# Performance work log

Hardware: AMD Instinct MI355X
Metric: run time of the kernel (lower is better)

## Reference

```python
import jax, jax.numpy as jnp
import numpy as np


def setup_inputs() -> dict:
    key = jax.random.key(0)
    k1, k2, k3 = jax.random.split(key, 3)
    B, S, IN, OUT = 4, 2048, 4096, 4096
    # int8 activations, weights, bias (stored as int8; math accumulates in int32)
    x = jax.random.randint(k1, (B, S, IN), -127, 128, dtype=jnp.int32).astype(jnp.int8)
    weight = jax.random.randint(k2, (OUT, IN), -127, 128, dtype=jnp.int32).astype(jnp.int8)  # (out, in)
    bias = jax.random.randint(k3, (1, OUT), -127, 128, dtype=jnp.int32).astype(jnp.int8)
    alpha = jnp.float32(0.001)  # input_scale*weight_scale/output_scale
    beta = jnp.float32(0.01)    # bias_scale/output_scale
    return {"x": x, "weight": weight, "bias": bias, "alpha": alpha, "beta": beta}


def reference(x, weight, bias, alpha, beta):
    # Flatten leading dims: (B,S,IN) -> (N,IN)
    x_shape = x.shape
    xf = x.reshape(-1, x_shape[-1])
    acc = jax.lax.dot_general(
        xf, weight,
        dimension_numbers=(((1,), (1,)), ((), ())),
        preferred_element_type=jnp.int32,
    )  # (N, OUT) int32
    # Fused epilogue: y = round(alpha*acc + beta*bias), saturate to int8
    yf = alpha * acc.astype(jnp.float32) + beta * bias.astype(jnp.float32)
    y = jnp.clip(jnp.round(yf), -128.0, 127.0).astype(jnp.int8)
    return y.reshape(*x_shape[:-1], -1)
```

## Files before the change

### kernel.cpp

```cpp
#include <hip/hip_runtime.h>
#include <stdint.h>

using i32x4  = __attribute__((ext_vector_type(4)))  int;
using i32x16 = __attribute__((ext_vector_type(16))) int;

#define M_TOT 8192
#define N_TOT 4096
#define K_TOT 4096
#define BM 256
#define BN 256

__device__ __forceinline__ void gload_lds16(const void* g, void* l) {
  __builtin_amdgcn_global_load_lds(
      (const __attribute__((address_space(1))) void*)(uintptr_t)g,
      (__attribute__((address_space(3))) void*)(uint32_t)(uintptr_t)l,
      16, 0, 0);
}

__global__ void pack_tiles(const int* __restrict__ a32, const int* __restrict__ b32,
                           int8_t* __restrict__ ap, int8_t* __restrict__ bp,
                           int na, int ntot) {
  int stride = gridDim.x * blockDim.x;
  for (int idx = blockIdx.x * blockDim.x + threadIdx.x; idx < ntot; idx += stride) {
    int i = idx;
    const int* src;
    int8_t* dst;
    if (idx < na) { src = a32; dst = ap; }
    else          { src = b32; dst = bp; i = idx - na; }
    int sp = i & 3;
    int rr = (i >> 2) & 255;
    int kc = (i >> 10) & 63;
    int p  = i >> 16;
    int sl = sp ^ ((rr >> 1) & 3);
    const i32x4* s = (const i32x4*)(src + (((size_t)(p * 256 + rr)) << 12) + kc * 64 + sl * 16);
    i32x4 a = s[0], b = s[1], c = s[2], d = s[3];
    i32x4 o;
    o.x = (a.x & 255) | ((a.y & 255) << 8) | ((a.z & 255) << 16) | (a.w << 24);
    o.y = (b.x & 255) | ((b.y & 255) << 8) | ((b.z & 255) << 16) | (b.w << 24);
    o.z = (c.x & 255) | ((c.y & 255) << 8) | ((c.z & 255) << 16) | (c.w << 24);
    o.w = (d.x & 255) | ((d.y & 255) << 8) | ((d.z & 255) << 16) | (d.w << 24);
    ((i32x4*)dst)[i] = o;
  }
}

#define STAGE_A(KC, SLOT) {                                                 \
    const int8_t* _g = Asrc + (size_t)(KC) * 16384 + stoff;                 \
    char* _d = lds + (SLOT) * 16384 + stoff;                                \
    gload_lds16(_g, _d); gload_lds16(_g + 8192, _d + 8192); }
#define STAGE_B(KC, SLOT) {                                                 \
    const int8_t* _g = Bsrc + (size_t)(KC) * 16384 + stoff;                 \
    char* _d = lds + 32768 + (SLOT) * 16384 + stoff;                        \
    gload_lds16(_g, _d); gload_lds16(_g + 8192, _d + 8192); }

#define LOAD_SET(FA, FB, SLOT, KS) {                                        \
    const char* _pa = lds + (SLOT) * 16384 + kOff[KS];                      \
    const char* _pb = _pa + 32768;                                          \
    FA[0] = *(const i32x4*)(_pa + aRow[0]);                                 \
    FA[1] = *(const i32x4*)(_pa + aRow[1]);                                 \
    FA[2] = *(const i32x4*)(_pa + aRow[2]);                                 \
    FA[3] = *(const i32x4*)(_pa + aRow[3]);                                 \
    FB[0] = *(const i32x4*)(_pb + bRow[0]);                                 \
    FB[1] = *(const i32x4*)(_pb + bRow[1]); }

#define MFMA8(FA, FB)                                                       \
    _Pragma("unroll")                                                       \
    for (int mi = 0; mi < 4; ++mi)                                          \
    _Pragma("unroll")                                                       \
    for (int ni = 0; ni < 2; ++ni)                                          \
      acc[mi][ni] = __builtin_amdgcn_mfma_i32_32x32x32_i8(FA[mi], FB[ni], acc[mi][ni], 0, 0, 0);

#define KTILE(SA_, SB_, SC_, SLOT, KC2, DO_STAGE, DO_NEXT) {                \
    LOAD_SET(fA##SB_, fB##SB_, SLOT, 1)                                     \
    asm volatile("s_waitcnt vmcnt(0)" ::: "memory");                        \
    __builtin_amdgcn_s_barrier();                                           \
    __builtin_amdgcn_sched_barrier(0);                                      \
    if (DO_STAGE) { STAGE_A(KC2, SLOT) STAGE_B(KC2, SLOT) }                 \
    __builtin_amdgcn_s_setprio(1);                                          \
    MFMA8(fA##SA_, fB##SA_)                                                 \
    __builtin_amdgcn_s_setprio(0);                                          \
    if (DO_NEXT) LOAD_SET(fA##SC_, fB##SC_, (SLOT) ^ 1, 0)                  \
    __builtin_amdgcn_s_setprio(1);                                          \
    MFMA8(fA##SB_, fB##SB_)                                                 \
    __builtin_amdgcn_s_setprio(0); }

__global__ __launch_bounds__(512, 2) void gemm_w8a8(
    const int8_t* __restrict__ Apack,
    const int8_t* __restrict__ Bpack,
    const int*    __restrict__ bias,
    const float*  __restrict__ alphap,
    const float*  __restrict__ betap,
    int* __restrict__ out)
{
  __shared__ __align__(16) char lds[65536];

  const int bid = blockIdx.x;
  const int xcd = bid & 7, wi = bid >> 3;
  const int tm = (xcd & 3) * 8 + (wi & 7);
  const int tn = (xcd >> 2) * 8 + (wi >> 3);

  const int tid = threadIdx.x;
  const int w   = tid >> 6;
  const int l   = tid & 63;
  const int lr  = l & 31;
  const int hi  = l >> 5;
  const int wr  = w >> 2;
  const int wc  = w & 3;
  const int stoff = tid * 16;

  const int8_t* Asrc = Apack + ((size_t)tm << 20);
  const int8_t* Bsrc = Bpack + ((size_t)tn << 20);

  const int swz = (lr >> 1) & 3;
  int aRow[4], bRow[2], kOff[2];
#pragma unroll
  for (int mi = 0; mi < 4; ++mi) aRow[mi] = (wr * 128 + mi * 32 + lr) * 64;
#pragma unroll
  for (int ni = 0; ni < 2; ++ni) bRow[ni] = (wc * 64 + ni * 32 + lr) * 64;
#pragma unroll
  for (int ks = 0; ks < 2; ++ks) kOff[ks] = ((((ks << 1) | hi)) ^ swz) * 16;

  i32x16 acc[4][2] = {};
  i32x4 fA0[4], fB0[2], fA1[4], fB1[2], fA2[4], fB2[2];

  STAGE_A(0, 0) STAGE_B(0, 0)
  STAGE_A(1, 1) STAGE_B(1, 1)
  asm volatile("s_waitcnt vmcnt(4)" ::: "memory");
  __builtin_amdgcn_s_barrier();
  __builtin_amdgcn_sched_barrier(0);
  LOAD_SET(fA0, fB0, 0, 0)

  for (int t = 0; t < 10; ++t) {
    const int kk = t * 6;
    KTILE(0, 1, 2, 0, kk + 2, 1, 1)
    KTILE(2, 0, 1, 1, kk + 3, 1, 1)
    KTILE(1, 2, 0, 0, kk + 4, 1, 1)
    KTILE(0, 1, 2, 1, kk + 5, 1, 1)
    KTILE(2, 0, 1, 0, kk + 6, 1, 1)
    KTILE(1, 2, 0, 1, kk + 7, 1, 1)
  }
  KTILE(0, 1, 2, 0, 62, 1, 1)
  KTILE(2, 0, 1, 1, 63, 1, 1)
  KTILE(1, 2, 0, 0, 0,  0, 1)
  KTILE(0, 1, 2, 1, 0,  0, 0)

  const float alpha = *alphap;
  const float beta  = *betap;
  const int brow = tm * BM, bcol = tn * BN;
#pragma unroll
  for (int ni = 0; ni < 2; ++ni) {
    const int col = bcol + wc * 64 + ni * 32 + lr;
    const float bb = beta * (float)bias[col];
#pragma unroll
    for (int mi = 0; mi < 4; ++mi) {
      const int rbase = brow + wr * 128 + mi * 32 + 4 * hi;
#pragma unroll
      for (int r = 0; r < 16; ++r) {
        const int row = rbase + (r & 3) + 8 * (r >> 2);
        float v = alpha * (float)acc[mi][ni][r] + bb;
        v = rintf(v);
        v = fminf(127.f, fmaxf(-128.f, v));
        out[(size_t)row * N_TOT + col] = (int)v;
      }
    }
  }
}

extern "C" void kernel_launch(void* const* d_in, const int* in_sizes, int n_in,
                              void* d_out, int out_size, void* d_ws, size_t ws_size,
                              hipStream_t stream) {
  const int*   x32    = (const int*)d_in[0];
  const int*   w32    = (const int*)d_in[1];
  const int*   bias   = (const int*)d_in[2];
  const float* alphap = (const float*)d_in[3];
  const float* betap  = (const float*)d_in[4];
  int* out = (int*)d_out;

  int8_t* xp = (int8_t*)d_ws;
  int8_t* wp = xp + (size_t)M_TOT * K_TOT;

  const int na   = (M_TOT * K_TOT) / 16;
  const int ntot = na + (N_TOT * K_TOT) / 16;
  pack_tiles<<<3072, 256, 0, stream>>>(x32, w32, xp, wp, na, ntot);

  gemm_w8a8<<<512, 512, 0, stream>>>(xp, wp, bias, alphap, betap, out);
}
```

Measured before the change: 197.5 us.

## Split warps into two phase-offset groups with triple-buffered LDS staging

Moves LDS staging from a double buffer to a triple buffer and regroups the 8 waves into two parity groups of four. One group loads its whole k-tile fragments from LDS and then runs MFMAs. The other group runs MFMAs on fragments it prefetched during the previous interval and then loads the next tile. The aim is to keep the matrix units busy by having one group issue LDS reads while the other computes. It raises LDS use to 96KB per block and changes the per-wave tile mapping, which could cut occupancy or add register pressure, and the divergent per-wave schedule may not line up as intended.

```diff
diff --git a/kernel.cpp b/kernel.cpp
--- a/kernel.cpp
+++ b/kernel.cpp
@@ -43,45 +43,45 @@
   }
 }
 
-#define STAGE_A(KC, SLOT) {                                                 \
-    const int8_t* _g = Asrc + (size_t)(KC) * 16384 + stoff;                 \
-    char* _d = lds + (SLOT) * 16384 + stoff;                                \
-    gload_lds16(_g, _d); gload_lds16(_g + 8192, _d + 8192); }
-#define STAGE_B(KC, SLOT) {                                                 \
-    const int8_t* _g = Bsrc + (size_t)(KC) * 16384 + stoff;                 \
-    char* _d = lds + 32768 + (SLOT) * 16384 + stoff;                        \
-    gload_lds16(_g, _d); gload_lds16(_g + 8192, _d + 8192); }
+#define STAGE_AB(KC, SLOT) {                                                \
+    const int8_t* _ga = Asrc + (size_t)(KC) * 16384 + stoff;                \
+    char* _da = lds + (SLOT) * 16384 + stoff;                               \
+    gload_lds16(_ga, _da); gload_lds16(_ga + 8192, _da + 8192);             \
+    const int8_t* _gb = Bsrc + (size_t)(KC) * 16384 + stoff;                \
+    char* _db = lds + 49152 + (SLOT) * 16384 + stoff;                       \
+    gload_lds16(_gb, _db); gload_lds16(_gb + 8192, _db + 8192); }
 
-#define LOAD_SET(FA, FB, SLOT, KS) {                                        \
-    const char* _pa = lds + (SLOT) * 16384 + kOff[KS];                      \
-    const char* _pb = _pa + 32768;                                          \
-    FA[0] = *(const i32x4*)(_pa + aRow[0]);                                 \
-    FA[1] = *(const i32x4*)(_pa + aRow[1]);                                 \
-    FA[2] = *(const i32x4*)(_pa + aRow[2]);                                 \
-    FA[3] = *(const i32x4*)(_pa + aRow[3]);                                 \
-    FB[0] = *(const i32x4*)(_pb + bRow[0]);                                 \
-    FB[1] = *(const i32x4*)(_pb + bRow[1]); }
+#define LOAD_TILE(FA, FB, SLOT) {                                           \
+    const char* _p0 = lds + (SLOT) * 16384;                                 \
+    _Pragma("unroll") for (int ks = 0; ks < 2; ++ks) {                      \
+      _Pragma("unroll") for (int mi = 0; mi < 4; ++mi)                      \
+        FA[ks][mi] = *(const i32x4*)(_p0 + aRow[mi] + kOff[ks]);            \
+      _Pragma("unroll") for (int ni = 0; ni < 2; ++ni)                      \
+        FB[ks][ni] = *(const i32x4*)(_p0 + 49152 + bRow[ni] + kOff[ks]);    \
+    } }
 
-#define MFMA8(FA, FB)                                                       \
-    _Pragma("unroll")                                                       \
-    for (int mi = 0; mi < 4; ++mi)                                          \
-    _Pragma("unroll")                                                       \
-    for (int ni = 0; ni < 2; ++ni)                                          \
-      acc[mi][ni] = __builtin_amdgcn_mfma_i32_32x32x32_i8(FA[mi], FB[ni], acc[mi][ni], 0, 0, 0);
+#define MFMA16(FA, FB)                                                      \
+    _Pragma("unroll") for (int ks = 0; ks < 2; ++ks)                        \
+    _Pragma("unroll") for (int mi = 0; mi < 4; ++mi)                        \
+    _Pragma("unroll") for (int ni = 0; ni < 2; ++ni)                        \
+      acc[mi][ni] = __builtin_amdgcn_mfma_i32_32x32x32_i8(FA[ks][mi], FB[ks][ni], acc[mi][ni], 0, 0, 0);
 
-#define KTILE(SA_, SB_, SC_, SLOT, KC2, DO_STAGE, DO_NEXT) {                \
-    LOAD_SET(fA##SB_, fB##SB_, SLOT, 1)                                     \
+#define INTERVAL(SLOT, NSLOT, SP, SR, KC2, DO_STAGE, DO_AHEAD) {            \
     asm volatile("s_waitcnt vmcnt(0)" ::: "memory");                        \
     __builtin_amdgcn_s_barrier();                                           \
     __builtin_amdgcn_sched_barrier(0);                                      \
-    if (DO_STAGE) { STAGE_A(KC2, SLOT) STAGE_B(KC2, SLOT) }                 \
-    __builtin_amdgcn_s_setprio(1);                                          \
-    MFMA8(fA##SA_, fB##SA_)                                                 \
-    __builtin_amdgcn_s_setprio(0);                                          \
-    if (DO_NEXT) LOAD_SET(fA##SC_, fB##SC_, (SLOT) ^ 1, 0)                  \
-    __builtin_amdgcn_s_setprio(1);                                          \
-    MFMA8(fA##SB_, fB##SB_)                                                 \
-    __builtin_amdgcn_s_setprio(0); }
+    if (DO_STAGE) STAGE_AB(KC2, (KC2) % 3)                                  \
+    if (!par) {                                                             \
+      LOAD_TILE(fA##SP, fB##SP, SLOT)                                       \
+      __builtin_amdgcn_s_setprio(1);                                        \
+      MFMA16(fA##SP, fB##SP)                                                \
+      __builtin_amdgcn_s_setprio(0);                                        \
+    } else {                                                                \
+      __builtin_amdgcn_s_setprio(1);                                        \
+      MFMA16(fA##SP, fB##SP)                                                \
+      __builtin_amdgcn_s_setprio(0);                                        \
+      if (DO_AHEAD) LOAD_TILE(fA##SR, fB##SR, NSLOT)                        \
+    } }
 
 __global__ __launch_bounds__(512, 2) void gemm_w8a8(
     const int8_t* __restrict__ Apack,
@@ -91,7 +91,7 @@
     const float*  __restrict__ betap,
     int* __restrict__ out)
 {
-  __shared__ __align__(16) char lds[65536];
+  __shared__ __align__(16) char lds[98304];
 
   const int bid = blockIdx.x;
   const int xcd = bid & 7, wi = bid >> 3;
@@ -103,8 +103,9 @@
   const int l   = tid & 63;
   const int lr  = l & 31;
   const int hi  = l >> 5;
-  const int wr  = w >> 2;
-  const int wc  = w & 3;
+  const int wr  = w & 1;
+  const int wc  = (w >> 1) & 3;
+  const int par = w >> 2;
   const int stoff = tid * 16;
 
   const int8_t* Asrc = Apack + ((size_t)tm << 20);
@@ -120,28 +121,28 @@
   for (int ks = 0; ks < 2; ++ks) kOff[ks] = ((((ks << 1) | hi)) ^ swz) * 16;
 
   i32x16 acc[4][2] = {};
-  i32x4 fA0[4], fB0[2], fA1[4], fB1[2], fA2[4], fB2[2];
+  i32x4 fA0[2][4], fB0[2][2], fA1[2][4], fB1[2][2];
 
-  STAGE_A(0, 0) STAGE_B(0, 0)
-  STAGE_A(1, 1) STAGE_B(1, 1)
+  STAGE_AB(0, 0)
+  STAGE_AB(1, 1)
   asm volatile("s_waitcnt vmcnt(4)" ::: "memory");
   __builtin_amdgcn_s_barrier();
   __builtin_amdgcn_sched_barrier(0);
-  LOAD_SET(fA0, fB0, 0, 0)
+  if (par) LOAD_TILE(fA0, fB0, 0)
 
   for (int t = 0; t < 10; ++t) {
     const int kk = t * 6;
-    KTILE(0, 1, 2, 0, kk + 2, 1, 1)
-    KTILE(2, 0, 1, 1, kk + 3, 1, 1)
-    KTILE(1, 2, 0, 0, kk + 4, 1, 1)
-    KTILE(0, 1, 2, 1, kk + 5, 1, 1)
-    KTILE(2, 0, 1, 0, kk + 6, 1, 1)
-    KTILE(1, 2, 0, 1, kk + 7, 1, 1)
+    INTERVAL(0, 1, 0, 1, kk + 2, 1, 1)
+    INTERVAL(1, 2, 1, 0, kk + 3, 1, 1)
+    INTERVAL(2, 0, 0, 1, kk + 4, 1, 1)
+    INTERVAL(0, 1, 1, 0, kk + 5, 1, 1)
+    INTERVAL(1, 2, 0, 1, kk + 6, 1, 1)
+    INTERVAL(2, 0, 1, 0, kk + 7, 1, 1)
   }
-  KTILE(0, 1, 2, 0, 62, 1, 1)
-  KTILE(2, 0, 1, 1, 63, 1, 1)
-  KTILE(1, 2, 0, 0, 0,  0, 1)
-  KTILE(0, 1, 2, 1, 0,  0, 0)
+  INTERVAL(0, 1, 0, 1, 62, 1, 1)
+  INTERVAL(1, 2, 1, 0, 63, 1, 1)
+  INTERVAL(2, 0, 0, 1, 0,  0, 1)
+  INTERVAL(0, 1, 1, 0, 0,  0, 0)
 
   const float alpha = *alphap;
   const float beta  = *betap;
```

New measurement: 336.6 us. 1.7x slower.

## Load B fragments directly to registers with fragment-ordered packing, triple-buffer A in LDS

Applied to the files above, without the earlier changes.

The pack kernel now writes B in an MFMA-fragment order, so each wave can read its B operands straight from global memory into registers and skip LDS staging for B. A stays in LDS and becomes triple-buffered across 48KB, and each interval issues all its A fragment reads at once instead of the previous interleaved LOAD_SET pipeline. This cuts LDS traffic and shared-memory use, but exposes global-load latency on B and raises register pressure from three B register sets.

```diff
diff --git a/kernel.cpp b/kernel.cpp
--- a/kernel.cpp
+++ b/kernel.cpp
@@ -22,17 +22,32 @@
                            int na, int ntot) {
   int stride = gridDim.x * blockDim.x;
   for (int idx = blockIdx.x * blockDim.x + threadIdx.x; idx < ntot; idx += stride) {
-    int i = idx;
     const int* src;
     int8_t* dst;
-    if (idx < na) { src = a32; dst = ap; }
-    else          { src = b32; dst = bp; i = idx - na; }
-    int sp = i & 3;
-    int rr = (i >> 2) & 255;
-    int kc = (i >> 10) & 63;
-    int p  = i >> 16;
-    int sl = sp ^ ((rr >> 1) & 3);
-    const i32x4* s = (const i32x4*)(src + (((size_t)(p * 256 + rr)) << 12) + kc * 64 + sl * 16);
+    size_t selem;
+    int i;
+    if (idx < na) {
+      i = idx; src = a32; dst = ap;
+      int sp = i & 3;
+      int rr = (i >> 2) & 255;
+      int kc = (i >> 10) & 63;
+      int p  = i >> 16;
+      int sl = sp ^ ((rr >> 1) & 3);
+      selem = (((size_t)(p * 256 + rr)) << 12) + kc * 64 + sl * 16;
+    } else {
+      i = idx - na; src = b32; dst = bp;
+      int lr = i & 31;
+      int hi = (i >> 5) & 1;
+      int ks = (i >> 6) & 1;
+      int ni = (i >> 7) & 1;
+      int wc = (i >> 8) & 3;
+      int kc = (i >> 10) & 63;
+      int pn = i >> 16;
+      int row = pn * 256 + wc * 64 + ni * 32 + lr;
+      int kb  = kc * 64 + ks * 32 + hi * 16;
+      selem = (size_t)row * 4096 + kb;
+    }
+    const i32x4* s = (const i32x4*)(src + selem);
     i32x4 a = s[0], b = s[1], c = s[2], d = s[3];
     i32x4 o;
     o.x = (a.x & 255) | ((a.y & 255) << 8) | ((a.z & 255) << 16) | (a.w << 24);
@@ -47,40 +62,28 @@
     const int8_t* _g = Asrc + (size_t)(KC) * 16384 + stoff;                 \
     char* _d = lds + (SLOT) * 16384 + stoff;                                \
     gload_lds16(_g, _d); gload_lds16(_g + 8192, _d + 8192); }
-#define STAGE_B(KC, SLOT) {                                                 \
-    const int8_t* _g = Bsrc + (size_t)(KC) * 16384 + stoff;                 \
-    char* _d = lds + 32768 + (SLOT) * 16384 + stoff;                        \
-    gload_lds16(_g, _d); gload_lds16(_g + 8192, _d + 8192); }
 
-#define LOAD_SET(FA, FB, SLOT, KS) {                                        \
-    const char* _pa = lds + (SLOT) * 16384 + kOff[KS];                      \
-    const char* _pb = _pa + 32768;                                          \
-    FA[0] = *(const i32x4*)(_pa + aRow[0]);                                 \
-    FA[1] = *(const i32x4*)(_pa + aRow[1]);                                 \
-    FA[2] = *(const i32x4*)(_pa + aRow[2]);                                 \
-    FA[3] = *(const i32x4*)(_pa + aRow[3]);                                 \
-    FB[0] = *(const i32x4*)(_pb + bRow[0]);                                 \
-    FB[1] = *(const i32x4*)(_pb + bRow[1]); }
+#define BLOAD(KC, SET) {                                                    \
+    const int8_t* _b = Bw + (size_t)(KC) * 16384;                           \
+    Bs##SET[0][0] = *(const i32x4*)(_b);                                    \
+    Bs##SET[0][1] = *(const i32x4*)(_b + 1024);                             \
+    Bs##SET[1][0] = *(const i32x4*)(_b + 2048);                             \
+    Bs##SET[1][1] = *(const i32x4*)(_b + 3072); }
 
-#define MFMA8(FA, FB)                                                       \
-    _Pragma("unroll")                                                       \
-    for (int mi = 0; mi < 4; ++mi)                                          \
-    _Pragma("unroll")                                                       \
-    for (int ni = 0; ni < 2; ++ni)                                          \
-      acc[mi][ni] = __builtin_amdgcn_mfma_i32_32x32x32_i8(FA[mi], FB[ni], acc[mi][ni], 0, 0, 0);
-
-#define KTILE(SA_, SB_, SC_, SLOT, KC2, DO_STAGE, DO_NEXT) {                \
-    LOAD_SET(fA##SB_, fB##SB_, SLOT, 1)                                     \
-    asm volatile("s_waitcnt vmcnt(0)" ::: "memory");                        \
+#define INTERVAL(SLOT, NS, VM, KC2, DO) {                                   \
+    asm volatile("s_waitcnt vmcnt(" VM ")" ::: "memory");                   \
     __builtin_amdgcn_s_barrier();                                           \
     __builtin_amdgcn_sched_barrier(0);                                      \
-    if (DO_STAGE) { STAGE_A(KC2, SLOT) STAGE_B(KC2, SLOT) }                 \
+    if (DO) { STAGE_A(KC2, NS) BLOAD(KC2, NS) }                             \
+    { const char* _pa = lds + (SLOT) * 16384;                               \
+      _Pragma("unroll") for (int ks = 0; ks < 2; ++ks)                      \
+      _Pragma("unroll") for (int mi = 0; mi < 4; ++mi)                      \
+        Af[ks][mi] = *(const i32x4*)(_pa + aRow[mi] + kOff[ks]); }          \
     __builtin_amdgcn_s_setprio(1);                                          \
-    MFMA8(fA##SA_, fB##SA_)                                                 \
-    __builtin_amdgcn_s_setprio(0);                                          \
-    if (DO_NEXT) LOAD_SET(fA##SC_, fB##SC_, (SLOT) ^ 1, 0)                  \
-    __builtin_amdgcn_s_setprio(1);                                          \
-    MFMA8(fA##SB_, fB##SB_)                                                 \
+    _Pragma("unroll") for (int ks = 0; ks < 2; ++ks)                        \
+    _Pragma("unroll") for (int mi = 0; mi < 4; ++mi)                        \
+    _Pragma("unroll") for (int ni = 0; ni < 2; ++ni)                        \
+      acc[mi][ni] = __builtin_amdgcn_mfma_i32_32x32x32_i8(Af[ks][mi], Bs##SLOT[ni][ks], acc[mi][ni], 0, 0, 0); \
     __builtin_amdgcn_s_setprio(0); }
 
 __global__ __launch_bounds__(512, 2) void gemm_w8a8(
@@ -91,7 +94,7 @@
     const float*  __restrict__ betap,
     int* __restrict__ out)
 {
-  __shared__ __align__(16) char lds[65536];
+  __shared__ __align__(16) char lds[49152];
 
   const int bid = blockIdx.x;
   const int xcd = bid & 7, wi = bid >> 3;
@@ -108,40 +111,34 @@
   const int stoff = tid * 16;
 
   const int8_t* Asrc = Apack + ((size_t)tm << 20);
-  const int8_t* Bsrc = Bpack + ((size_t)tn << 20);
+  const int8_t* Bw   = Bpack + ((size_t)tn << 20) + wc * 4096 + l * 16;
 
   const int swz = (lr >> 1) & 3;
-  int aRow[4], bRow[2], kOff[2];
+  int aRow[4], kOff[2];
 #pragma unroll
   for (int mi = 0; mi < 4; ++mi) aRow[mi] = (wr * 128 + mi * 32 + lr) * 64;
-#pragma unroll
-  for (int ni = 0; ni < 2; ++ni) bRow[ni] = (wc * 64 + ni * 32 + lr) * 64;
 #pragma unroll
   for (int ks = 0; ks < 2; ++ks) kOff[ks] = ((((ks << 1) | hi)) ^ swz) * 16;
 
   i32x16 acc[4][2] = {};
-  i32x4 fA0[4], fB0[2], fA1[4], fB1[2], fA2[4], fB2[2];
+  i32x4 Af[2][4];
+  i32x4 Bs0[2][2], Bs1[2][2], Bs2[2][2];
 
-  STAGE_A(0, 0) STAGE_B(0, 0)
-  STAGE_A(1, 1) STAGE_B(1, 1)
-  asm volatile("s_waitcnt vmcnt(4)" ::: "memory");
-  __builtin_amdgcn_s_barrier();
+  STAGE_A(0, 0) BLOAD(0, 0)
   __builtin_amdgcn_sched_barrier(0);
-  LOAD_SET(fA0, fB0, 0, 0)
+  STAGE_A(1, 1) BLOAD(1, 1)
+  __builtin_amdgcn_sched_barrier(0);
 
-  for (int t = 0; t < 10; ++t) {
-    const int kk = t * 6;
-    KTILE(0, 1, 2, 0, kk + 2, 1, 1)
-    KTILE(2, 0, 1, 1, kk + 3, 1, 1)
-    KTILE(1, 2, 0, 0, kk + 4, 1, 1)
-    KTILE(0, 1, 2, 1, kk + 5, 1, 1)
-    KTILE(2, 0, 1, 0, kk + 6, 1, 1)
-    KTILE(1, 2, 0, 1, kk + 7, 1, 1)
+  INTERVAL(0, 2, "6", 2, 1)
+  for (int t = 0; t < 20; ++t) {
+    const int kk = t * 3;
+    INTERVAL(1, 0, "6", kk + 3, 1)
+    INTERVAL(2, 1, "6", kk + 4, 1)
+    INTERVAL(0, 2, "6", kk + 5, 1)
   }
-  KTILE(0, 1, 2, 0, 62, 1, 1)
-  KTILE(2, 0, 1, 1, 63, 1, 1)
-  KTILE(1, 2, 0, 0, 0,  0, 1)
-  KTILE(0, 1, 2, 1, 0,  0, 0)
+  INTERVAL(1, 0, "6", 63, 1)
+  INTERVAL(2, 1, "6", 0, 0)
+  INTERVAL(0, 2, "0", 0, 0)
 
   const float alpha = *alphap;
   const float beta  = *betap;
```

Result: slower. 206.4 us (+4.5%).

## Use 4-wave blocks with 128x128 warp tiles and 128-wide K double-buffered stages

Applied to the files above, without the earlier changes.

Cuts the workgroup from 8 waves to 4. Each wave now computes a 128x128 output tile (4x4 MFMA accumulators), which doubles per-wave fragment reuse. Each pipeline interval stages a 128-deep K chunk (32KB per operand) into a 128KB double-buffered LDS region, so there are fewer barriers per K step. Explicit sched_group_barrier hints interleave the LDS reads, global-to-LDS loads and MFMAs. The trade-off is lower occupancy (one block per CU), higher register pressure from 256 accumulator VGPRs, and more LDS per block.

```diff
diff --git a/kernel.cpp b/kernel.cpp
--- a/kernel.cpp
+++ b/kernel.cpp
@@ -43,47 +43,62 @@
   }
 }
 
-#define STAGE_A(KC, SLOT) {                                                 \
-    const int8_t* _g = Asrc + (size_t)(KC) * 16384 + stoff;                 \
-    char* _d = lds + (SLOT) * 16384 + stoff;                                \
-    gload_lds16(_g, _d); gload_lds16(_g + 8192, _d + 8192); }
-#define STAGE_B(KC, SLOT) {                                                 \
-    const int8_t* _g = Bsrc + (size_t)(KC) * 16384 + stoff;                 \
-    char* _d = lds + 32768 + (SLOT) * 16384 + stoff;                        \
-    gload_lds16(_g, _d); gload_lds16(_g + 8192, _d + 8192); }
+#define STAGE2(I, S) {                                                      \
+    const int8_t* _ga = Asrc + ((size_t)(I) << 15) + stoff;                 \
+    char* _da = lds + (S) * 32768 + stoff;                                  \
+    gload_lds16(_ga,          _da);          gload_lds16(_ga + 4096,  _da + 4096);  \
+    gload_lds16(_ga + 8192,   _da + 8192);   gload_lds16(_ga + 12288, _da + 12288); \
+    gload_lds16(_ga + 16384,  _da + 16384);  gload_lds16(_ga + 20480, _da + 20480); \
+    gload_lds16(_ga + 24576,  _da + 24576);  gload_lds16(_ga + 28672, _da + 28672); \
+    const int8_t* _gb = Bsrc + ((size_t)(I) << 15) + stoff;                 \
+    char* _db = lds + 65536 + (S) * 32768 + stoff;                          \
+    gload_lds16(_gb,          _db);          gload_lds16(_gb + 4096,  _db + 4096);  \
+    gload_lds16(_gb + 8192,   _db + 8192);   gload_lds16(_gb + 12288, _db + 12288); \
+    gload_lds16(_gb + 16384,  _db + 16384);  gload_lds16(_gb + 20480, _db + 20480); \
+    gload_lds16(_gb + 24576,  _db + 24576);  gload_lds16(_gb + 28672, _db + 28672); }
 
-#define LOAD_SET(FA, FB, SLOT, KS) {                                        \
-    const char* _pa = lds + (SLOT) * 16384 + kOff[KS];                      \
-    const char* _pb = _pa + 32768;                                          \
-    FA[0] = *(const i32x4*)(_pa + aRow[0]);                                 \
-    FA[1] = *(const i32x4*)(_pa + aRow[1]);                                 \
-    FA[2] = *(const i32x4*)(_pa + aRow[2]);                                 \
-    FA[3] = *(const i32x4*)(_pa + aRow[3]);                                 \
-    FB[0] = *(const i32x4*)(_pb + bRow[0]);                                 \
-    FB[1] = *(const i32x4*)(_pb + bRow[1]); }
+#define LOAD_SET(SET, S, KS) {                                              \
+    const char* _pa = lds + (S) * 32768 + kOff[KS];                         \
+    const char* _pb = _pa + 65536;                                          \
+    Af##SET[0] = *(const i32x4*)(_pa + aRow[0]);                            \
+    Af##SET[1] = *(const i32x4*)(_pa + aRow[1]);                            \
+    Af##SET[2] = *(const i32x4*)(_pa + aRow[2]);                            \
+    Af##SET[3] = *(const i32x4*)(_pa + aRow[3]);                            \
+    Bf##SET[0] = *(const i32x4*)(_pb + bRow[0]);                            \
+    Bf##SET[1] = *(const i32x4*)(_pb + bRow[1]);                            \
+    Bf##SET[2] = *(const i32x4*)(_pb + bRow[2]);                            \
+    Bf##SET[3] = *(const i32x4*)(_pb + bRow[3]); }
 
-#define MFMA8(FA, FB)                                                       \
-    _Pragma("unroll")                                                       \
-    for (int mi = 0; mi < 4; ++mi)                                          \
-    _Pragma("unroll")                                                       \
-    for (int ni = 0; ni < 2; ++ni)                                          \
-      acc[mi][ni] = __builtin_amdgcn_mfma_i32_32x32x32_i8(FA[mi], FB[ni], acc[mi][ni], 0, 0, 0);
+#define MFMA16(SET)                                                         \
+    _Pragma("unroll") for (int mi = 0; mi < 4; ++mi)                        \
+    _Pragma("unroll") for (int ni = 0; ni < 4; ++ni)                        \
+      acc[mi][ni] = __builtin_amdgcn_mfma_i32_32x32x32_i8(Af##SET[mi], Bf##SET[ni], acc[mi][ni], 0, 0, 0);
 
-#define KTILE(SA_, SB_, SC_, SLOT, KC2, DO_STAGE, DO_NEXT) {                \
-    LOAD_SET(fA##SB_, fB##SB_, SLOT, 1)                                     \
+#define SGB(m, n) __builtin_amdgcn_sched_group_barrier((m), (n), 0)
+#define PAIR SGB(0x100, 1); SGB(0x8, 2);
+#define PAIR8 PAIR PAIR PAIR PAIR PAIR PAIR PAIR PAIR
+
+#define INTERVAL(I, S, DO_STAGE) {                                          \
     asm volatile("s_waitcnt vmcnt(0)" ::: "memory");                        \
     __builtin_amdgcn_s_barrier();                                           \
     __builtin_amdgcn_sched_barrier(0);                                      \
-    if (DO_STAGE) { STAGE_A(KC2, SLOT) STAGE_B(KC2, SLOT) }                 \
+    if (DO_STAGE) STAGE2((I) + 1, (S) ^ 1)                                  \
+    LOAD_SET(0, S, 0)                                                       \
+    LOAD_SET(1, S, 1)                                                       \
     __builtin_amdgcn_s_setprio(1);                                          \
-    MFMA8(fA##SA_, fB##SA_)                                                 \
+    MFMA16(0)                                                               \
+    LOAD_SET(2, S, 2)                                                       \
+    MFMA16(1)                                                               \
+    LOAD_SET(0, S, 3)                                                       \
+    MFMA16(2)                                                               \
+    MFMA16(0)                                                               \
     __builtin_amdgcn_s_setprio(0);                                          \
-    if (DO_NEXT) LOAD_SET(fA##SC_, fB##SC_, (SLOT) ^ 1, 0)                  \
-    __builtin_amdgcn_s_setprio(1);                                          \
-    MFMA8(fA##SB_, fB##SB_)                                                 \
-    __builtin_amdgcn_s_setprio(0); }
+    SGB(0x10, 16);                                                          \
+    SGB(0x100, 8);                                                          \
+    PAIR8 PAIR8 PAIR8                                                       \
+    SGB(0x8, 16); }
 
-__global__ __launch_bounds__(512, 2) void gemm_w8a8(
+__global__ __launch_bounds__(256, 1) void gemm_w8a8(
     const int8_t* __restrict__ Apack,
     const int8_t* __restrict__ Bpack,
     const int*    __restrict__ bias,
@@ -91,7 +106,7 @@
     const float*  __restrict__ betap,
     int* __restrict__ out)
 {
-  __shared__ __align__(16) char lds[65536];
+  __shared__ __align__(16) char lds[131072];
 
   const int bid = blockIdx.x;
   const int xcd = bid & 7, wi = bid >> 3;
@@ -103,52 +118,42 @@
   const int l   = tid & 63;
   const int lr  = l & 31;
   const int hi  = l >> 5;
-  const int wr  = w >> 2;
-  const int wc  = w & 3;
+  const int wr  = w >> 1;
+  const int wc  = w & 1;
   const int stoff = tid * 16;
 
   const int8_t* Asrc = Apack + ((size_t)tm << 20);
   const int8_t* Bsrc = Bpack + ((size_t)tn << 20);
 
   const int swz = (lr >> 1) & 3;
-  int aRow[4], bRow[2], kOff[2];
+  int aRow[4], bRow[4], kOff[4];
 #pragma unroll
   for (int mi = 0; mi < 4; ++mi) aRow[mi] = (wr * 128 + mi * 32 + lr) * 64;
 #pragma unroll
-  for (int ni = 0; ni < 2; ++ni) bRow[ni] = (wc * 64 + ni * 32 + lr) * 64;
+  for (int ni = 0; ni < 4; ++ni) bRow[ni] = (wc * 128 + ni * 32 + lr) * 64;
 #pragma unroll
-  for (int ks = 0; ks < 2; ++ks) kOff[ks] = ((((ks << 1) | hi)) ^ swz) * 16;
+  for (int ks = 0; ks < 4; ++ks)
+    kOff[ks] = (ks >> 1) * 16384 + (((((ks & 1) << 1) | hi)) ^ swz) * 16;
 
-  i32x16 acc[4][2] = {};
-  i32x4 fA0[4], fB0[2], fA1[4], fB1[2], fA2[4], fB2[2];
+  i32x16 acc[4][4] = {};
+  i32x4 Af0[4], Bf0[4], Af1[4], Bf1[4], Af2[4], Bf2[4];
 
-  STAGE_A(0, 0) STAGE_B(0, 0)
-  STAGE_A(1, 1) STAGE_B(1, 1)
-  asm volatile("s_waitcnt vmcnt(4)" ::: "memory");
-  __builtin_amdgcn_s_barrier();
-  __builtin_amdgcn_sched_barrier(0);
-  LOAD_SET(fA0, fB0, 0, 0)
+  STAGE2(0, 0)
 
-  for (int t = 0; t < 10; ++t) {
-    const int kk = t * 6;
-    KTILE(0, 1, 2, 0, kk + 2, 1, 1)
-    KTILE(2, 0, 1, 1, kk + 3, 1, 1)
-    KTILE(1, 2, 0, 0, kk + 4, 1, 1)
-    KTILE(0, 1, 2, 1, kk + 5, 1, 1)
-    KTILE(2, 0, 1, 0, kk + 6, 1, 1)
-    KTILE(1, 2, 0, 1, kk + 7, 1, 1)
+  for (int t = 0; t < 15; ++t) {
+    const int I = t * 2;
+    INTERVAL(I + 0, 0, 1)
+    INTERVAL(I + 1, 1, 1)
   }
-  KTILE(0, 1, 2, 0, 62, 1, 1)
-  KTILE(2, 0, 1, 1, 63, 1, 1)
-  KTILE(1, 2, 0, 0, 0,  0, 1)
-  KTILE(0, 1, 2, 1, 0,  0, 0)
+  INTERVAL(30, 0, 1)
+  INTERVAL(31, 1, 0)
 
   const float alpha = *alphap;
   const float beta  = *betap;
   const int brow = tm * BM, bcol = tn * BN;
 #pragma unroll
-  for (int ni = 0; ni < 2; ++ni) {
-    const int col = bcol + wc * 64 + ni * 32 + lr;
+  for (int ni = 0; ni < 4; ++ni) {
+    const int col = bcol + wc * 128 + ni * 32 + lr;
     const float bb = beta * (float)bias[col];
 #pragma unroll
     for (int mi = 0; mi < 4; ++mi) {
@@ -182,5 +187,5 @@
   const int ntot = na + (N_TOT * K_TOT) / 16;
   pack_tiles<<<3072, 256, 0, stream>>>(x32, w32, xp, wp, na, ntot);
 
-  gemm_w8a8<<<512, 512, 0, stream>>>(xp, wp, bias, alphap, betap, out);
+  gemm_w8a8<<<512, 256, 0, stream>>>(xp, wp, bias, alphap, betap, out);
 }
```

New measurement: 202.4 us. +2.5%, slower.
